# Performance work log

Measured on AMD Instinct MI355X. Metric: run time of the kernel, lower is better.

The kernel has to match this reference:

```python
import jax, jax.numpy as jnp
import numpy as np

N_NET, D, N_H, N_T, N_IN, N_OUT = 1, 4, 8, 2048, 256, 256


def setup_inputs() -> dict:
    key = jax.random.key(0)
    k1, k2, k3 = jax.random.split(key, 3)
    r_prime = jax.random.normal(k1, (N_NET, D, N_T, N_IN), dtype=jnp.float32)
    # learned params per __init__: E ~ N(0, 0.02), Q ~ N(0, 0.02)
    E = 0.02 * jax.random.normal(k2, (N_NET, N_H, N_OUT, N_IN), dtype=jnp.float32)
    Q = 0.02 * jax.random.normal(k3, (N_NET, N_H, N_IN, N_IN), dtype=jnp.float32)
    return {"r_prime": r_prime, "E": E, "Q": Q}


def reference(r_prime, E, Q):
    n_t = r_prime.shape[2]
    # Omega[N,b,h,t,u] = r'[N,b,t,i] Q[N,h,i,j] r'[N,b,u,j]  (bilinear scores, no softmax)
    Omega = jnp.einsum('Nbti,Nhij,Nbuj->Nbhtu', r_prime, Q, r_prime)
    mask = jnp.tril(jnp.ones((n_t, n_t), dtype=Omega.dtype))  # causal lower-triangular
    Omega = Omega * mask
    # r[N,b,t,i] = Omega[N,b,h,t,u] E[N,h,i,j] r'[N,b,u,j]
    r = jnp.einsum('Nbhtu,Nhij,Nbuj->Nbti', Omega, E, r_prime)
    return r
```

## Files before the change

### kernel.cpp

```cpp
#include <hip/hip_runtime.h>
#include <stdint.h>

typedef unsigned short u16;
typedef __attribute__((ext_vector_type(4))) float f32x4;
typedef __attribute__((ext_vector_type(4))) uint32_t u32x4;
typedef __attribute__((ext_vector_type(8))) __bf16 bf16x8;

#define B_ 4
#define H_ 8
#define T_ 2048
#define C_ 256
#define KC 2048
#define NCH 32
#define XP 528
#define SP 144

static __device__ __forceinline__ f32x4 mfma16(u32x4 a, u32x4 b, f32x4 c) {
  union { u32x4 u; bf16x8 b; } A, Bb;
  A.u = a; Bb.u = b;
  return __builtin_amdgcn_mfma_f32_16x16x32_bf16(A.b, Bb.b, c, 0, 0, 0);
}
static __device__ __forceinline__ u16 f2b(float f) {
  union { __bf16 h; u16 u; } r; r.h = (__bf16)f; return r.u;
}

__global__ __launch_bounds__(256) void k_prep(const float* __restrict__ rp_f,
                                              const float* __restrict__ E_f,
                                              const float* __restrict__ Q_f,
                                              u16* __restrict__ rbf,
                                              u16* __restrict__ rpT,
                                              u16* __restrict__ qtb,
                                              u16* __restrict__ ec) {
  __shared__ u16 l[64][72];
  const int r = blockIdx.x, tid = threadIdx.x;
  if (r < 512) {
    const int b = r >> 7, i0 = ((r >> 5) & 3) * 64, t0 = (r & 31) * 64;
    const int tj = tid & 63, tq = tid >> 6;
    const float* src = rp_f + (size_t)b * T_ * C_;
    u16* rb = rbf + (size_t)b * T_ * C_;
    #pragma unroll
    for (int rr = 0; rr < 16; ++rr) {
      int tl = rr * 4 + tq;
      u16 v = f2b(src[(size_t)(t0 + tl) * C_ + i0 + tj]);
      l[tl][tj] = v;
      rb[(size_t)(t0 + tl) * C_ + i0 + tj] = v;
    }
    __syncthreads();
    u16* dst = rpT + (size_t)b * C_ * T_;
    #pragma unroll
    for (int rr = 0; rr < 16; ++rr) {
      int il = rr * 4 + tq;
      dst[(size_t)(i0 + il) * T_ + t0 + tj] = l[tj][il];
    }
  } else if (r < 640) {
    const int q = r - 512;
    const int h = q >> 4, i0 = ((q >> 2) & 3) * 64, j0 = (q & 3) * 64;
    const int tj = tid & 63, tq = tid >> 6;
    const float* qh = Q_f + (size_t)h * C_ * C_;
    #pragma unroll
    for (int rr = 0; rr < 16; ++rr) {
      int i = rr * 4 + tq;
      l[i][tj] = f2b(qh[(size_t)(i0 + i) * C_ + j0 + tj]);
    }
    __syncthreads();
    u16* qth = qtb + (size_t)h * C_ * C_;
    #pragma unroll
    for (int rr = 0; rr < 16; ++rr) {
      int j = rr * 4 + tq;
      qth[(size_t)(j0 + j) * C_ + i0 + tj] = l[tj][j];
    }
  } else {
    const int q = r - 640;
    size_t e = ((size_t)q * 256 + tid) * 4;
    int h = (int)(e >> 16), i = (int)((e >> 8) & 255), j = (int)(e & 255);
    f32x4 v = *(const f32x4*)(E_f + e);
    union { u16 h4[4]; uint64_t qq; } p;
    #pragma unroll
    for (int c = 0; c < 4; ++c) p.h4[c] = f2b(v[c]);
    *(uint64_t*)(ec + (size_t)i * KC + h * 256 + j) = p.qq;
  }
}

__global__ __launch_bounds__(256) void k_gram(const u16* __restrict__ rpT,
                                              u16* __restrict__ G) {
  __shared__ u16 gls[4][16][20];
  const int js = blockIdx.x, iq = blockIdx.y, b = blockIdx.z;
  const int tid = threadIdx.x, lane = tid & 63, v = tid >> 6;
  const int l15 = lane & 15, lq = lane >> 4;
  const u16* rtb = rpT + (size_t)b * C_ * T_;
  const int irow = 64 * iq + 16 * v;
  const int rrow = lane >> 2, rc4 = (lane & 3) * 4;

  f32x4 acc = (f32x4)0.f;

  for (int k = 0; k < NCH; ++k) {
    #pragma unroll
    for (int rr = 0; rr < 4; ++rr)
      gls[v][4 * lq + rr][l15] = f2b(acc[rr]);
    __builtin_amdgcn_wave_barrier();
    u16* gk = G + (size_t)(b * NCH + k) * C_ * C_;
    *(uint64_t*)(gk + (size_t)(irow + rrow) * C_ + 16 * js + rc4) =
        *(const uint64_t*)&gls[v][rrow][rc4];
    __builtin_amdgcn_wave_barrier();

    u32x4 am[2], bn[2];
    #pragma unroll
    for (int kk = 0; kk < 2; ++kk) {
      am[kk] = *(const u32x4*)(rtb + (size_t)(irow + l15) * T_ +
                               64 * k + 32 * kk + 8 * lq);
      bn[kk] = *(const u32x4*)(rtb + (size_t)(16 * js + l15) * T_ +
                               64 * k + 32 * kk + 8 * lq);
    }
    #pragma unroll
    for (int kk = 0; kk < 2; ++kk)
      acc = mfma16(am[kk], bn[kk], acc);
  }
}

__global__ __launch_bounds__(512, 2) void k_z(const u16* __restrict__ rbf,
                                              const u16* __restrict__ rpT,
                                              const u16* __restrict__ qtb,
                                              const u16* __restrict__ G,
                                              u16* __restrict__ ZC) {
  __shared__ __align__(16) char smem[119808];
  char* rp_l = smem;
  char* x0   = smem + 33792;
  char* x1   = smem + 67584;
  char* s0   = smem + 101376;
  char* s1   = smem + 110592;

  const int tile = blockIdx.x, b = blockIdx.y, hg = blockIdx.z;
  const int t0 = tile * 64;
  const int tid = threadIdx.x, lane = tid & 63, w = tid >> 6;
  const int l15 = lane & 15, lq = lane >> 4;
  const int mh = w >> 2, nq = w & 3;

  const u16* rpb = rbf + (size_t)b * T_ * C_;
  const u16* rtb = rpT + (size_t)b * C_ * T_;
  const u16* gt  = G + (size_t)(b * NCH + tile) * C_ * C_;
  const u16* qth0 = qtb + (size_t)(2 * hg) * C_ * C_;
  const u16* qth1 = qtb + (size_t)(2 * hg + 1) * C_ * C_;

  {
    const int row = tid >> 3, seg = tid & 7;
    const char* src = (const char*)(rpb + (size_t)(t0 + row) * C_);
    #pragma unroll
    for (int c = 0; c < 4; ++c) {
      u32x4 vv = *(const u32x4*)(src + seg * 64 + c * 16);
      *(u32x4*)(rp_l + (size_t)row * XP + seg * 64 + c * 16) = vv;
    }
  }
  __syncthreads();

  #pragma unroll
  for (int nn = 0; nn < 2; ++nn) {
    const int nt = 2 * w + nn;
    u32x4 bq0[8], bq1[8];
    #pragma unroll
    for (int kk = 0; kk < 8; ++kk) {
      bq0[kk] = *(const u32x4*)(qth0 + (size_t)(16 * nt + l15) * C_ +
                                32 * kk + 8 * lq);
      bq1[kk] = *(const u32x4*)(qth1 + (size_t)(16 * nt + l15) * C_ +
                                32 * kk + 8 * lq);
    }
    #pragma unroll
    for (int mm = 0; mm < 4; ++mm) {
      u32x4 am[8];
      #pragma unroll
      for (int kk = 0; kk < 8; ++kk)
        am[kk] = *(const u32x4*)(rp_l + (size_t)(16 * mm + l15) * XP +
                                 64 * kk + 16 * lq);
      f32x4 q0 = (f32x4)0.f, q1 = (f32x4)0.f;
      #pragma unroll
      for (int kk = 0; kk < 8; ++kk) {
        q0 = mfma16(am[kk], bq0[kk], q0);
        q1 = mfma16(am[kk], bq1[kk], q1);
      }
      #pragma unroll
      for (int rr = 0; rr < 4; ++rr) {
        size_t off = (size_t)(16 * mm + 4 * lq + rr) * XP + (16 * nt + l15) * 2;
        *(u16*)(x0 + off) = f2b(q0[rr]);
        *(u16*)(x1 + off) = f2b(q1[rr]);
      }
    }
  }
  __syncthreads();

  f32x4 a0[2][4], a1[2][4];
  #pragma unroll
  for (int m = 0; m < 2; ++m)
    #pragma unroll
    for (int n = 0; n < 4; ++n) { a0[m][n] = (f32x4)0.f; a1[m][n] = (f32x4)0.f; }

  #pragma unroll
  for (int n = 0; n < 4; ++n) {
    const int nt = 4 * nq + n;
    u32x4 bg[8];
    #pragma unroll
    for (int kk = 0; kk < 8; ++kk)
      bg[kk] = *(const u32x4*)(gt + (size_t)(16 * nt + l15) * C_ +
                               32 * kk + 8 * lq);
    #pragma unroll
    for (int m = 0; m < 2; ++m) {
      const size_t roff = (size_t)(16 * (2 * mh + m) + l15) * XP;
      u32x4 qa0[8], qa1[8];
      #pragma unroll
      for (int kk = 0; kk < 8; ++kk) {
        qa0[kk] = *(const u32x4*)(x0 + roff + 64 * kk + 16 * lq);
        qa1[kk] = *(const u32x4*)(x1 + roff + 64 * kk + 16 * lq);
      }
      #pragma unroll
      for (int kk = 0; kk < 8; ++kk) {
        a0[m][n] = mfma16(qa0[kk], bg[kk], a0[m][n]);
        a1[m][n] = mfma16(qa1[kk], bg[kk], a1[m][n]);
      }
    }
  }

  {
    const int ms = w & 3;
    const char* xs = (w >> 2) ? x1 : x0;
    char* ss = (w >> 2) ? s1 : s0;
    u32x4 qa3[8];
    #pragma unroll
    for (int kk = 0; kk < 8; ++kk)
      qa3[kk] = *(const u32x4*)(xs + (size_t)(16 * ms + l15) * XP +
                                64 * kk + 16 * lq);
    #pragma unroll
    for (int un = 0; un < 4; ++un) {
      u32x4 bs[8];
      #pragma unroll
      for (int kk = 0; kk < 8; ++kk)
        bs[kk] = *(const u32x4*)(rp_l + (size_t)(16 * un + l15) * XP +
                                 64 * kk + 16 * lq);
      f32x4 sacc = (f32x4)0.f;
      #pragma unroll
      for (int kk = 0; kk < 8; ++kk) sacc = mfma16(qa3[kk], bs[kk], sacc);
      #pragma unroll
      for (int rr = 0; rr < 4; ++rr) {
        int tl = 16 * ms + 4 * lq + rr;
        int ul = 16 * un + l15;
        float sv = (ul > tl) ? 0.f : sacc[rr];
        *(u16*)(ss + (size_t)tl * SP + ul * 2) = f2b(sv);
      }
    }
  }
  __syncthreads();

  {
    u32x4 sa0[2][2], sa1[2][2];
    #pragma unroll
    for (int m = 0; m < 2; ++m)
      #pragma unroll
      for (int kk = 0; kk < 2; ++kk) {
        size_t off = (size_t)(16 * (2 * mh + m) + l15) * SP + 64 * kk + 16 * lq;
        sa0[m][kk] = *(const u32x4*)(s0 + off);
        sa1[m][kk] = *(const u32x4*)(s1 + off);
      }
    #pragma unroll
    for (int n = 0; n < 4; ++n) {
      const int nt = 4 * nq + n;
      #pragma unroll
      for (int kk = 0; kk < 2; ++kk) {
        u32x4 vb = *(const u32x4*)(rtb + (size_t)(16 * nt + l15) * T_ +
                                   t0 + 32 * kk + 8 * lq);
        #pragma unroll
        for (int m = 0; m < 2; ++m) {
          a0[m][n] = mfma16(sa0[m][kk], vb, a0[m][n]);
          a1[m][n] = mfma16(sa1[m][kk], vb, a1[m][n]);
        }
      }
    }
  }

  #pragma unroll
  for (int m = 0; m < 2; ++m)
    #pragma unroll
    for (int n = 0; n < 4; ++n)
      #pragma unroll
      for (int rr = 0; rr < 4; ++rr) {
        size_t off = (size_t)(16 * (2 * mh + m) + 4 * lq + rr) * XP +
                     (16 * (4 * nq + n) + l15) * 2;
        *(u16*)(x0 + off) = f2b(a0[m][n][rr]);
        *(u16*)(x1 + off) = f2b(a1[m][n][rr]);
      }
  __syncthreads();

  {
    const int row = tid >> 3, seg = tid & 7;
    char* d0 = (char*)(ZC + ((size_t)(b * T_ + t0 + row) * KC + (2 * hg) * 256));
    char* d1 = (char*)(ZC + ((size_t)(b * T_ + t0 + row) * KC + (2 * hg + 1) * 256));
    #pragma unroll
    for (int c = 0; c < 4; ++c) {
      u32x4 v0 = *(const u32x4*)(x0 + (size_t)row * XP + seg * 64 + c * 16);
      u32x4 v1 = *(const u32x4*)(x1 + (size_t)row * XP + seg * 64 + c * 16);
      *(u32x4*)(d0 + seg * 64 + c * 16) = v0;
      *(u32x4*)(d1 + seg * 64 + c * 16) = v1;
    }
  }
}

__global__ __launch_bounds__(256) void k_o(const u16* __restrict__ ZC,
                                           const u16* __restrict__ ec,
                                           float* __restrict__ out) {
  const int mt = blockIdx.x, b = blockIdx.y;
  const int tid = threadIdx.x, lane = tid & 63, v = tid >> 6;
  const int l15 = lane & 15, lq = lane >> 4;

  const u16* za_b = ZC + (size_t)(b * T_ + mt * 32) * KC;

  f32x4 acc[2][4];
  #pragma unroll
  for (int m = 0; m < 2; ++m)
    #pragma unroll
    for (int n = 0; n < 4; ++n) acc[m][n] = (f32x4)0.f;

  #pragma unroll 2
  for (int kk = 0; kk < 64; ++kk) {
    u32x4 am[2], bn[4];
    #pragma unroll
    for (int m = 0; m < 2; ++m)
      am[m] = *(const u32x4*)(za_b + (size_t)(16 * m + l15) * KC +
                              32 * kk + 8 * lq);
    #pragma unroll
    for (int n = 0; n < 4; ++n)
      bn[n] = *(const u32x4*)(ec + (size_t)(64 * v + 16 * n + l15) * KC +
                              32 * kk + 8 * lq);
    #pragma unroll
    for (int m = 0; m < 2; ++m)
      #pragma unroll
      for (int n = 0; n < 4; ++n)
        acc[m][n] = mfma16(am[m], bn[n], acc[m][n]);
  }

  float* ob = out + ((size_t)b * T_ + mt * 32) * C_;
  #pragma unroll
  for (int m = 0; m < 2; ++m)
    #pragma unroll
    for (int n = 0; n < 4; ++n)
      #pragma unroll
      for (int rr = 0; rr < 4; ++rr)
        ob[(size_t)(16 * m + 4 * lq + rr) * C_ + 64 * v + 16 * n + l15] =
            acc[m][n][rr];
}

extern "C" void kernel_launch(void* const* d_in, const int* in_sizes, int n_in,
                              void* d_out, int out_size, void* d_ws, size_t ws_size,
                              hipStream_t stream) {
  (void)ws_size; (void)out_size;
  const float* rp_f = nullptr;
  const float* sm[2] = {nullptr, nullptr};
  int ns = 0;
  for (int i = 0; i < n_in; ++i) {
    if (in_sizes[i] == 2097152) {
      rp_f = (const float*)d_in[i];
    } else if (ns < 2) {
      sm[ns++] = (const float*)d_in[i];
    }
  }
  const float* E_f = sm[0];
  const float* Q_f = sm[1];

  const size_t MB = 1024 * 1024;
  u16* G   = (u16*)d_ws;
  u16* rbf = (u16*)((char*)d_ws + 16 * MB);
  u16* rpT = (u16*)((char*)d_ws + 20 * MB);
  u16* qtb = (u16*)((char*)d_ws + 24 * MB);
  u16* ec  = (u16*)((char*)d_ws + 25 * MB);
  u16* ZC  = (u16*)((char*)d_ws + 26 * MB);
  float* outf = (float*)d_out;

  k_prep<<<1152, 256, 0, stream>>>(rp_f, E_f, Q_f, rbf, rpT, qtb, ec);
  k_gram<<<dim3(16, 4, 4), 256, 0, stream>>>(rpT, G);
  k_z<<<dim3(32, 4, 4), 512, 0, stream>>>(rbf, rpT, qtb, G, ZC);
  k_o<<<dim3(64, 4), 256, 0, stream>>>(ZC, ec, outf);
}
```

Before: 130.3 us.

## Fuse E projection into k_z epilogue and reduce head-group partials separately

Measured after the change: 120.2 us. 7.8% less time.

```diff
diff --git a/kernel.cpp b/kernel.cpp
--- a/kernel.cpp
+++ b/kernel.cpp
@@ -121,7 +121,8 @@
                                               const u16* __restrict__ rpT,
                                               const u16* __restrict__ qtb,
                                               const u16* __restrict__ G,
-                                              u16* __restrict__ ZC) {
+                                              const u16* __restrict__ ec,
+                                              float* __restrict__ part) {
   __shared__ __align__(16) char smem[119808];
   char* rp_l = smem;
   char* x0   = smem + 33792;
@@ -287,61 +288,59 @@
   __syncthreads();
 
   {
-    const int row = tid >> 3, seg = tid & 7;
-    char* d0 = (char*)(ZC + ((size_t)(b * T_ + t0 + row) * KC + (2 * hg) * 256));
-    char* d1 = (char*)(ZC + ((size_t)(b * T_ + t0 + row) * KC + (2 * hg + 1) * 256));
-    #pragma unroll
-    for (int c = 0; c < 4; ++c) {
-      u32x4 v0 = *(const u32x4*)(x0 + (size_t)row * XP + seg * 64 + c * 16);
-      u32x4 v1 = *(const u32x4*)(x1 + (size_t)row * XP + seg * 64 + c * 16);
-      *(u32x4*)(d0 + seg * 64 + c * 16) = v0;
-      *(u32x4*)(d1 + seg * 64 + c * 16) = v1;
-    }
-  }
-}
-
-__global__ __launch_bounds__(256) void k_o(const u16* __restrict__ ZC,
-                                           const u16* __restrict__ ec,
-                                           float* __restrict__ out) {
-  const int mt = blockIdx.x, b = blockIdx.y;
-  const int tid = threadIdx.x, lane = tid & 63, v = tid >> 6;
-  const int l15 = lane & 15, lq = lane >> 4;
-
-  const u16* za_b = ZC + (size_t)(b * T_ + mt * 32) * KC;
-
-  f32x4 acc[2][4];
-  #pragma unroll
-  for (int m = 0; m < 2; ++m)
-    #pragma unroll
-    for (int n = 0; n < 4; ++n) acc[m][n] = (f32x4)0.f;
-
-  #pragma unroll 2
-  for (int kk = 0; kk < 64; ++kk) {
-    u32x4 am[2], bn[4];
+    const u16* e0 = ec + (size_t)(2 * hg) * 256;
+    const u16* e1 = ec + (size_t)(2 * hg + 1) * 256;
+    f32x4 oa[2][4];
     #pragma unroll
     for (int m = 0; m < 2; ++m)
-      am[m] = *(const u32x4*)(za_b + (size_t)(16 * m + l15) * KC +
-                              32 * kk + 8 * lq);
-    #pragma unroll
-    for (int n = 0; n < 4; ++n)
-      bn[n] = *(const u32x4*)(ec + (size_t)(64 * v + 16 * n + l15) * KC +
-                              32 * kk + 8 * lq);
+      #pragma unroll
+      for (int n = 0; n < 4; ++n) oa[m][n] = (f32x4)0.f;
+
+    #pragma unroll
+    for (int m = 0; m < 2; ++m) {
+      const size_t roff = (size_t)(16 * (2 * mh + m) + l15) * XP;
+      u32x4 za0[8], za1[8];
+      #pragma unroll
+      for (int kk = 0; kk < 8; ++kk) {
+        za0[kk] = *(const u32x4*)(x0 + roff + 64 * kk + 16 * lq);
+        za1[kk] = *(const u32x4*)(x1 + roff + 64 * kk + 16 * lq);
+      }
+      #pragma unroll
+      for (int n = 0; n < 4; ++n) {
+        const int irow = 64 * nq + 16 * n + l15;
+        u32x4 eb0[8], eb1[8];
+        #pragma unroll
+        for (int kk = 0; kk < 8; ++kk) {
+          eb0[kk] = *(const u32x4*)(e0 + (size_t)irow * KC + 32 * kk + 8 * lq);
+          eb1[kk] = *(const u32x4*)(e1 + (size_t)irow * KC + 32 * kk + 8 * lq);
+        }
+        #pragma unroll
+        for (int kk = 0; kk < 8; ++kk) {
+          oa[m][n] = mfma16(za0[kk], eb0[kk], oa[m][n]);
+          oa[m][n] = mfma16(za1[kk], eb1[kk], oa[m][n]);
+        }
+      }
+    }
+
+    float* pb = part + ((size_t)(hg * B_ + b) * T_ + t0) * C_;
     #pragma unroll
     for (int m = 0; m < 2; ++m)
       #pragma unroll
       for (int n = 0; n < 4; ++n)
-        acc[m][n] = mfma16(am[m], bn[n], acc[m][n]);
-  }
-
-  float* ob = out + ((size_t)b * T_ + mt * 32) * C_;
-  #pragma unroll
-  for (int m = 0; m < 2; ++m)
-    #pragma unroll
-    for (int n = 0; n < 4; ++n)
-      #pragma unroll
-      for (int rr = 0; rr < 4; ++rr)
-        ob[(size_t)(16 * m + 4 * lq + rr) * C_ + 64 * v + 16 * n + l15] =
-            acc[m][n][rr];
+        #pragma unroll
+        for (int rr = 0; rr < 4; ++rr)
+          pb[(size_t)(32 * mh + 16 * m + 4 * lq + rr) * C_ +
+             64 * nq + 16 * n + l15] = oa[m][n][rr];
+  }
+}
+
+__global__ __launch_bounds__(256) void k_final(const float* __restrict__ part,
+                                               float* __restrict__ out) {
+  const size_t idx = (size_t)blockIdx.x * 256 + threadIdx.x;
+  const size_t N = (size_t)B_ * T_ * C_ / 4;
+  const f32x4* p = (const f32x4*)part;
+  f32x4 s = p[idx] + p[N + idx] + p[2 * N + idx] + p[3 * N + idx];
+  ((f32x4*)out)[idx] = s;
 }
 
 extern "C" void kernel_launch(void* const* d_in, const int* in_sizes, int n_in,
@@ -367,11 +366,11 @@
   u16* rpT = (u16*)((char*)d_ws + 20 * MB);
   u16* qtb = (u16*)((char*)d_ws + 24 * MB);
   u16* ec  = (u16*)((char*)d_ws + 25 * MB);
-  u16* ZC  = (u16*)((char*)d_ws + 26 * MB);
+  float* part = (float*)((char*)d_ws + 26 * MB);
   float* outf = (float*)d_out;
 
   k_prep<<<1152, 256, 0, stream>>>(rp_f, E_f, Q_f, rbf, rpT, qtb, ec);
   k_gram<<<dim3(16, 4, 4), 256, 0, stream>>>(rpT, G);
-  k_z<<<dim3(32, 4, 4), 512, 0, stream>>>(rbf, rpT, qtb, G, ZC);
-  k_o<<<dim3(64, 4), 256, 0, stream>>>(ZC, ec, outf);
-}
+  k_z<<<dim3(32, 4, 4), 512, 0, stream>>>(rbf, rpT, qtb, G, ec, part);
+  k_final<<<2048, 256, 0, stream>>>(part, outf);
+}
```
